# Kernel tuning notes

Hardware: AMD Instinct MI355X
Metric: run time of the kernel (lower is better)

Reference implementation:

```python
import jax, jax.numpy as jnp
import numpy as np

EPS = 1e-9
# exp factors for iterations i = 4,3,2,1,0,-1,-2 ; i == -2 -> 0.0
EXP_FACTORS = np.array([-(4.0 ** i) if i != -2 else 0.0 for i in range(4, -3, -1)], dtype=np.float32)


def setup_inputs() -> dict:
    key = jax.random.key(0)
    k1, k2 = jax.random.split(key)
    B, N, D = 16, 2048, 256
    preds = jax.random.normal(k1, (B, N, D), dtype=jnp.float32)
    labels = jax.random.normal(k2, (B, N, D), dtype=jnp.float32)
    return {"preds": preds, "labels": labels}


def _pairwise_dist(p1, p2):
    # [B,N,1] + [B,1,N] - 2 * p1 @ p2^T -> [B,N,N]
    p1_norm = jnp.sum(p1 * p1, axis=-1)[..., :, None]
    p2_norm = jnp.sum(p2 * p2, axis=-1)[..., None, :]
    return p1_norm + p2_norm - 2.0 * jnp.einsum('bnd,bmd->bnm', p1, p2)


def _approx_match(pwdist):
    B, N, _ = pwdist.shape
    match0 = jnp.zeros_like(pwdist)
    currency0 = jnp.ones((B, N, 1), dtype=pwdist.dtype)
    cost0 = jnp.ones((B, 1, N), dtype=pwdist.dtype)

    def body(carry, exp_factor):
        match, cost, currency = carry
        bids = jnp.exp(exp_factor * pwdist) * cost              # [B,N,N]
        bids = bids * currency / (jnp.sum(bids, axis=2, keepdims=True) + EPS)
        bid_wt = jnp.minimum(cost / (jnp.sum(bids, axis=1, keepdims=True) + EPS), 1.0)
        bids = bids * bid_wt
        match = match + bids
        cost = jnp.maximum(cost - jnp.sum(bids, axis=1, keepdims=True), 0.0)
        currency = jnp.maximum(currency - jnp.sum(bids, axis=2, keepdims=True), 0.0)
        return (match, cost, currency), None

    (match, _, _), _ = jax.lax.scan(body, (match0, cost0, currency0), jnp.asarray(EXP_FACTORS))
    return match


def reference(preds, labels):
    pwdist = _pairwise_dist(preds, labels)
    match = _approx_match(pwdist)
    return jnp.sum(match * pwdist)
```

## Files before the change

kernel.cpp:

```cpp
#include <hip/hip_runtime.h>
#include <cstdint>

#define B_ 16
#define N_ 2048
#define D_ 256
#define EPS_ 1e-9f

#define AS1 __attribute__((address_space(1)))
#define AS3 __attribute__((address_space(3)))

typedef float f4 __attribute__((ext_vector_type(4)));
typedef float f16v __attribute__((ext_vector_type(16)));
typedef int v8i __attribute__((ext_vector_type(8)));

__device__ float blockReduceSum(float x, float* red){
  int tid = threadIdx.x;
  red[tid] = x; __syncthreads();
  #pragma unroll
  for (int off = 128; off > 0; off >>= 1){
    if (tid < off) red[tid] += red[tid + off];
    __syncthreads();
  }
  float r = red[0]; __syncthreads();
  return r;
}

__global__ __launch_bounds__(256) void prep_kernel(
    const float* __restrict__ preds, const float* __restrict__ labels,
    unsigned char* __restrict__ pa8, unsigned char* __restrict__ pb8,
    float* __restrict__ pn, float* __restrict__ ln,
    float* __restrict__ cost, float* __restrict__ currency,
    int* __restrict__ dmin, float* __restrict__ Ppart,
    float* __restrict__ npart, float* __restrict__ out){
  int s = blockIdx.y;
  int tid = threadIdx.x;
  if (s == 0){
    int i = blockIdx.x * 256 + tid;
    if (i < B_ * N_){ cost[i] = 1.f; currency[i] = 1.f; }
    if (i < B_) dmin[i] = 0x7f7fffff;
    if (i == 0) out[0] = 0.f;
  }
  const float* src = s ? labels : preds;
  unsigned char* dst = s ? pb8 : pa8;
  float* norms = s ? ln : pn;
  int w = tid >> 6, lane = tid & 63;
  size_t row0 = (size_t)blockIdx.x * 16 + (size_t)w * 4;
  float4 v[4];
  #pragma unroll
  for (int q = 0; q < 4; q++)
    v[q] = ((const float4*)(src + (row0 + q) * D_))[lane];
  __shared__ f4 part[4][64];
  __shared__ float nred[4];
  f4 s4;
  s4[0] = v[0].x + v[1].x + v[2].x + v[3].x;
  s4[1] = v[0].y + v[1].y + v[2].y + v[3].y;
  s4[2] = v[0].z + v[1].z + v[2].z + v[3].z;
  s4[3] = v[0].w + v[1].w + v[2].w + v[3].w;
  float nsum = 0.f;
  #pragma unroll
  for (int q = 0; q < 4; q++){
    float sum = v[q].x*v[q].x + v[q].y*v[q].y + v[q].z*v[q].z + v[q].w*v[q].w;
    #pragma unroll
    for (int off = 32; off >= 1; off >>= 1) sum += __shfl_xor(sum, off);
    if (lane == 0){ norms[row0 + q] = sum; nsum += sum; }
    int pk = 0;
    pk = __builtin_amdgcn_cvt_pk_fp8_f32(v[q].x, v[q].y, pk, false);
    pk = __builtin_amdgcn_cvt_pk_fp8_f32(v[q].z, v[q].w, pk, true);
    ((unsigned int*)(dst + (row0 + q) * D_))[lane] = (unsigned int)pk;
  }
  part[w][lane] = s4;
  if (lane == 0) nred[w] = nsum;
  __syncthreads();
  if (tid < 64){
    f4 t = part[0][tid];
    #pragma unroll
    for (int q = 1; q < 4; q++){
      t[0] += part[q][tid][0]; t[1] += part[q][tid][1];
      t[2] += part[q][tid][2]; t[3] += part[q][tid][3];
    }
    *(f4*)(Ppart + ((size_t)s * 2048 + blockIdx.x) * 256 + tid * 4) = t;
  }
  if (tid == 0)
    npart[s * 2048 + blockIdx.x] = nred[0] + nred[1] + nred[2] + nred[3];
}

__global__ __launch_bounds__(512, 4) void gemm_minmax(
    const unsigned char* __restrict__ pa, const unsigned char* __restrict__ pbm,
    const float* __restrict__ pn, const float* __restrict__ ln,
    int* __restrict__ dmin)
{
  int lid = blockIdx.x;
  int xcd = lid & 7;
  int l = lid >> 3;
  int b = 2 * xcd + (l >> 5);
  int p = l & 31;
  int tn = (p & 7) * 256;
  int tmb = (p >> 3) * 512;
  const unsigned char* A  = pa  + (size_t)b * N_ * D_;
  const unsigned char* Bm = pbm + (size_t)b * N_ * D_;
  __shared__ __align__(16) unsigned char smem[256 * 256];
  __shared__ float minred[8];
  unsigned char* Bs = smem;
  unsigned char* As0 = smem;
  unsigned char* As1 = smem + 16384;
  float* pnL = (float*)(smem + 32768);
  int tid = threadIdx.x, lane = tid & 63, w = tid >> 6;
  int wm = (w >> 2) * 32, wn = (w & 3) * 64;
  int l31 = lane & 31, half = lane >> 5;
  int rB = lane >> 4, cB = lane & 15;
  const int SC = 0x7F7F7F7F;

  #pragma unroll
  for (int q = 0; q < 8; q++){
    int R = q * 32 + w * 4;
    int r = R + rB;
    int gc = cB ^ (r & 7);
    __builtin_amdgcn_global_load_lds(
        (const AS1 unsigned int*)(const void*)&Bm[(size_t)(tn + r) * D_ + gc * 16],
        (AS3 unsigned int*)(void*)&Bs[R * 256 + lane * 16], 16, 0, 0);
  }

  float lnj[2];
  #pragma unroll
  for (int j = 0; j < 2; j++)
    lnj[j] = ln[(size_t)b * N_ + tn + wn + j * 32 + l31];

  __syncthreads();

  v8i bfr[2][4];
  #pragma unroll
  for (int j = 0; j < 2; j++){
    int rb = wn + j * 32 + l31;
    #pragma unroll
    for (int kc = 0; kc < 4; kc++){
      int c0 = kc * 4 + half * 2;
      int4 lo = *(const int4*)&Bs[rb * 256 + ((c0 ^ (rb & 7)) * 16)];
      int4 hi = *(const int4*)&Bs[rb * 256 + (((c0 + 1) ^ (rb & 7)) * 16)];
      v8i t;
      t[0] = lo.x; t[1] = lo.y; t[2] = lo.z; t[3] = lo.w;
      t[4] = hi.x; t[5] = hi.y; t[6] = hi.z; t[7] = hi.w;
      bfr[j][kc] = t;
    }
  }

  __syncthreads();

  __builtin_amdgcn_global_load_lds(
      (const AS1 unsigned int*)(const void*)&pn[(size_t)b * N_ + tmb + tid],
      (AS3 unsigned int*)(void*)&pnL[tid], 4, 0, 0);
  #pragma unroll
  for (int q = 0; q < 2; q++){
    int R = q * 32 + w * 4;
    int r = R + rB;
    int gc = cB ^ (r & 7);
    __builtin_amdgcn_global_load_lds(
        (const AS1 unsigned int*)(const void*)&A[(size_t)(tmb + r) * D_ + gc * 16],
        (AS3 unsigned int*)(void*)&As0[R * 256 + lane * 16], 16, 0, 0);
  }

  float mind = 3.4e38f;
  int buf = 0;
  for (int step = 0; step < 8; step++){
    __syncthreads();
    unsigned char* Acur = buf ? As1 : As0;
    unsigned char* Anxt = buf ? As0 : As1;
    if (step < 7){
      #pragma unroll
      for (int q = 0; q < 2; q++){
        int R = q * 32 + w * 4;
        int r = R + rB;
        int gc = cB ^ (r & 7);
        __builtin_amdgcn_global_load_lds(
            (const AS1 unsigned int*)(const void*)&A[(size_t)(tmb + (step + 1) * 64 + r) * D_ + gc * 16],
            (AS3 unsigned int*)(void*)&Anxt[R * 256 + lane * 16], 16, 0, 0);
      }
    }
    f16v acc[2];
    acc[0] = (f16v)0.f; acc[1] = (f16v)0.f;

    int ra = wm + l31;
    #pragma unroll
    for (int kc = 0; kc < 4; kc++){
      int c0 = kc * 4 + half * 2;
      int4 lo = *(const int4*)&Acur[ra * 256 + ((c0 ^ (ra & 7)) * 16)];
      int4 hi = *(const int4*)&Acur[ra * 256 + (((c0 + 1) ^ (ra & 7)) * 16)];
      v8i af;
      af[0] = lo.x; af[1] = lo.y; af[2] = lo.z; af[3] = lo.w;
      af[4] = hi.x; af[5] = hi.y; af[6] = hi.z; af[7] = hi.w;
      #pragma unroll
      for (int j = 0; j < 2; j++)
        acc[j] = __builtin_amdgcn_mfma_scale_f32_32x32x64_f8f6f4(
            af, bfr[j][kc], acc[j], 0, 0, 0, SC, 0, SC);
    }

    int prow0 = step * 64 + wm + half * 4;
    #pragma unroll
    for (int h = 0; h < 2; h++){
      float4 p0 = *(const float4*)&pnL[prow0 + h * 16];
      float4 p1 = *(const float4*)&pnL[prow0 + h * 16 + 8];
      float pv[8] = {p0.x, p0.y, p0.z, p0.w, p1.x, p1.y, p1.z, p1.w};
      #pragma unroll
      for (int j = 0; j < 2; j++){
        #pragma unroll
        for (int r8 = 0; r8 < 8; r8++){
          float v = pv[r8] + lnj[j] - 2.f * acc[j][h * 8 + r8];
          mind = fminf(mind, v);
        }
      }
    }
    buf ^= 1;
  }

  #pragma unroll
  for (int off = 32; off >= 1; off >>= 1) mind = fminf(mind, __shfl_xor(mind, off));
  if (lane == 0) minred[w] = mind;
  __syncthreads();
  if (tid == 0){
    float m = minred[0];
    #pragma unroll
    for (int q = 1; q < 8; q++) m = fminf(m, minred[q]);
    atomicMin(&dmin[b], __float_as_int(fmaxf(m, 0.f)));
  }
}

__global__ __launch_bounds__(256) void tail(
    const float* __restrict__ preds, const float* __restrict__ labels,
    const float* __restrict__ pn, const float* __restrict__ ln,
    float* __restrict__ cost, float* __restrict__ currency,
    const int* __restrict__ dmin, const float* __restrict__ Ppart,
    const float* __restrict__ npart, float* __restrict__ out)
{
  const float EF[6] = {-256.f, -64.f, -16.f, -4.f, -1.f, -0.25f};
  int b = blockIdx.x, tid = threadIdx.x;
  float dm = __int_as_float(dmin[b]);
  __shared__ float red[256];

  if (-0.25f * (dm - 16.f) < -55.f){
    float Pc = 0.f, Lc = 0.f;
    for (int k = 0; k < 128; k++){
      Pc += Ppart[((size_t)b * 128 + k) * 256 + tid];
      Lc += Ppart[((size_t)(2048 + b * 128 + k)) * 256 + tid];
    }
    float np = (tid < 128) ? npart[b * 128 + tid] : 0.f;
    float nl = (tid < 128) ? npart[2048 + b * 128 + tid] : 0.f;
    float Spn = blockReduceSum(np, red);
    float Sln = blockReduceSum(nl, red);
    float dot = blockReduceSum(Pc * Lc, red);
    if (tid == 0) atomicAdd(out, Spn + Sln - dot * (1.f / 1024.f));
    return;
  }

  __shared__ float alpha_l[N_];
  __shared__ float prow[D_];
  const float* A  = preds  + (size_t)b * N_ * D_;
  const float* Bm = labels + (size_t)b * N_ * D_;
  const float* pnb = pn + (size_t)b * N_;
  const float* lnb = ln + (size_t)b * N_;
  float* costb = cost + (size_t)b * N_;
  float* curb  = currency + (size_t)b * N_;
  for (int it = 0; it < 6; it++){
    float ef = EF[it];
    if (ef * (dm - 16.f) < -55.f) continue;
    float cost_c[8], colsum_c[8], bw_c[8], costnew_c[8];
    #pragma unroll
    for (int j = 0; j < 8; j++){ cost_c[j] = costb[j*256+tid]; colsum_c[j] = 0.f; }
    for (int r = 0; r < N_; r++){
      prow[tid] = A[(size_t)r * D_ + tid];
      __syncthreads();
      float s_c[8], rs = 0.f;
      for (int j = 0; j < 8; j++){
        int m = j*256+tid; float dot = 0.f;
        for (int k = 0; k < D_; k++) dot += prow[k] * Bm[(size_t)m * D_ + k];
        float d = pnb[r] + lnb[m] - 2.f*dot;
        float s = __expf(ef * d) * cost_c[j];
        s_c[j] = s; rs += s;
      }
      float tot = blockReduceSum(rs, red);
      float a = curb[r] / (tot + EPS_);
      if (tid == 0) alpha_l[r] = a;
      #pragma unroll
      for (int j = 0; j < 8; j++) colsum_c[j] += s_c[j] * a;
      __syncthreads();
    }
    #pragma unroll
    for (int j = 0; j < 8; j++){
      float cs = colsum_c[j];
      float bw = fminf(cost_c[j] / (cs + EPS_), 1.f);
      bw_c[j] = bw; costnew_c[j] = fmaxf(cost_c[j] - bw*cs, 0.f);
    }
    float contrib = 0.f;
    for (int r = 0; r < N_; r++){
      prow[tid] = A[(size_t)r * D_ + tid];
      __syncthreads();
      float a = alpha_l[r], rbs = 0.f;
      for (int j = 0; j < 8; j++){
        int m = j*256+tid; float dot = 0.f;
        for (int k = 0; k < D_; k++) dot += prow[k] * Bm[(size_t)m * D_ + k];
        float d = pnb[r] + lnb[m] - 2.f*dot;
        float bid = __expf(ef * d) * cost_c[j] * a * bw_c[j];
        rbs += bid; contrib += bid * d;
      }
      float tot = blockReduceSum(rbs, red);
      if (tid == 0) curb[r] = fmaxf(curb[r] - tot, 0.f);
      __syncthreads();
    }
    #pragma unroll
    for (int j = 0; j < 8; j++) costb[j*256+tid] = costnew_c[j];
    float ctot = blockReduceSum(contrib, red);
    if (tid == 0) atomicAdd(out, ctot);
    __syncthreads();
  }
  float s = 0.f;
  #pragma unroll
  for (int j = 0; j < 8; j++) s += costb[j*256+tid];
  float Sc = blockReduceSum(s, red);
  float sa = 0.f, spn = 0.f;
  #pragma unroll
  for (int j = 0; j < 8; j++){
    int i = j*256+tid;
    float a = curb[i] / (Sc + EPS_);
    alpha_l[i] = a; sa += a; spn += a * pnb[i];
  }
  float Sa  = blockReduceSum(sa, red);
  float Spn = blockReduceSum(spn, red);
  float Pc = 0.f;
  for (int r = 0; r < N_; r++)
    Pc += alpha_l[r] * A[(size_t)r * D_ + tid];
  __syncthreads();
  float sv = 0.f, sln = 0.f;
  #pragma unroll
  for (int j = 0; j < 8; j++){
    int i = j*256+tid;
    float c = costb[i];
    float bw = fminf(c / (c * Sa + EPS_), 1.f);
    float vv = c * bw;
    alpha_l[i] = vv; sv += vv; sln += vv * lnb[i];
  }
  float Sv  = blockReduceSum(sv, red);
  float Sln = blockReduceSum(sln, red);
  float Lc = 0.f;
  for (int m = 0; m < N_; m++)
    Lc += alpha_l[m] * Bm[(size_t)m * D_ + tid];
  float dot = blockReduceSum(Pc * Lc, red);
  if (tid == 0) atomicAdd(out, Spn * Sv + Sa * Sln - 2.f * dot);
}

extern "C" void kernel_launch(void* const* d_in, const int* in_sizes, int n_in,
                              void* d_out, int out_size, void* d_ws, size_t ws_size,
                              hipStream_t stream)
{
  const float* preds  = (const float*)d_in[0];
  const float* labels = (const float*)d_in[1];
  float* out = (float*)d_out;
  char* ws = (char*)d_ws;
  const size_t BN = (size_t)B_ * N_;
  size_t off = 0;
  float* cost     = (float*)(ws + off); off += BN * 4;
  float* currency = (float*)(ws + off); off += BN * 4;
  float* pn       = (float*)(ws + off); off += BN * 4;
  float* ln       = (float*)(ws + off); off += BN * 4;
  int*   dmin     = (int*)(ws + off);   off += 256;
  float* npart    = (float*)(ws + off); off += (size_t)2 * 2048 * 4;
  float* Ppart    = (float*)(ws + off); off += (size_t)2 * 2048 * 256 * 4;
  unsigned char* pa8 = (unsigned char*)(ws + off); off += BN * D_;
  unsigned char* pb8 = (unsigned char*)(ws + off); off += BN * D_;

  prep_kernel<<<dim3((unsigned)(BN / 16), 2), 256, 0, stream>>>(
      preds, labels, pa8, pb8, pn, ln, cost, currency, dmin, Ppart, npart, out);
  gemm_minmax<<<dim3(512), 512, 0, stream>>>(pa8, pb8, pn, ln, dmin);
  tail<<<dim3(B_), 256, 0, stream>>>(preds, labels, pn, ln, cost, currency, dmin,
                                     Ppart, npart, out);
}
```

Baseline: 141.8 us.

## Restructure fp8 min-distance GEMM: each wave owns one 32-col B slice, 32-row A steps

Reworks the work split in the fp8 MFMA min-distance kernel. Each of the 8 waves now holds a single 32-column B fragment and sweeps 32-row A tiles over 16 steps, instead of a 2x4 wave grid with two fragments and 64-row tiles. B and the A double buffers get separate LDS regions, so the extra sync that let them alias is gone. The pn row norms are now read straight from global memory instead of being staged in LDS. This cuts registers and syncs per step but doubles the number of pipeline steps, lowers MFMA work per barrier, and the larger 80 KB LDS footprint may cap occupancy below the 4 blocks per CU the launch bounds ask for.

```diff
diff --git a/kernel.cpp b/kernel.cpp
--- a/kernel.cpp
+++ b/kernel.cpp
@@ -98,14 +98,11 @@
   int tmb = (p >> 3) * 512;
   const unsigned char* A  = pa  + (size_t)b * N_ * D_;
   const unsigned char* Bm = pbm + (size_t)b * N_ * D_;
-  __shared__ __align__(16) unsigned char smem[256 * 256];
-  __shared__ float minred[8];
-  unsigned char* Bs = smem;
-  unsigned char* As0 = smem;
-  unsigned char* As1 = smem + 16384;
-  float* pnL = (float*)(smem + 32768);
+  __shared__ __align__(16) unsigned char smem[81920];
+  unsigned char* Bs  = smem;
+  unsigned char* As0 = smem + 65536;
+  unsigned char* As1 = smem + 65536 + 8192;
   int tid = threadIdx.x, lane = tid & 63, w = tid >> 6;
-  int wm = (w >> 2) * 32, wn = (w & 3) * 64;
   int l31 = lane & 31, half = lane >> 5;
   int rB = lane >> 4, cB = lane & 15;
   const int SC = 0x7F7F7F7F;
@@ -119,18 +116,21 @@
         (const AS1 unsigned int*)(const void*)&Bm[(size_t)(tn + r) * D_ + gc * 16],
         (AS3 unsigned int*)(void*)&Bs[R * 256 + lane * 16], 16, 0, 0);
   }
-
-  float lnj[2];
-  #pragma unroll
-  for (int j = 0; j < 2; j++)
-    lnj[j] = ln[(size_t)b * N_ + tn + wn + j * 32 + l31];
+  {
+    int r = w * 4 + rB;
+    int gc = cB ^ (r & 7);
+    __builtin_amdgcn_global_load_lds(
+        (const AS1 unsigned int*)(const void*)&A[(size_t)(tmb + r) * D_ + gc * 16],
+        (AS3 unsigned int*)(void*)&As0[(w * 4) * 256 + lane * 16], 16, 0, 0);
+  }
+
+  float lnr = ln[(size_t)b * N_ + tn + w * 32 + l31];
 
   __syncthreads();
 
-  v8i bfr[2][4];
-  #pragma unroll
-  for (int j = 0; j < 2; j++){
-    int rb = wn + j * 32 + l31;
+  v8i bfr[4];
+  {
+    int rb = w * 32 + l31;
     #pragma unroll
     for (int kc = 0; kc < 4; kc++){
       int c0 = kc * 4 + half * 2;
@@ -139,46 +139,25 @@
       v8i t;
       t[0] = lo.x; t[1] = lo.y; t[2] = lo.z; t[3] = lo.w;
       t[4] = hi.x; t[5] = hi.y; t[6] = hi.z; t[7] = hi.w;
-      bfr[j][kc] = t;
-    }
-  }
-
-  __syncthreads();
-
-  __builtin_amdgcn_global_load_lds(
-      (const AS1 unsigned int*)(const void*)&pn[(size_t)b * N_ + tmb + tid],
-      (AS3 unsigned int*)(void*)&pnL[tid], 4, 0, 0);
-  #pragma unroll
-  for (int q = 0; q < 2; q++){
-    int R = q * 32 + w * 4;
-    int r = R + rB;
-    int gc = cB ^ (r & 7);
-    __builtin_amdgcn_global_load_lds(
-        (const AS1 unsigned int*)(const void*)&A[(size_t)(tmb + r) * D_ + gc * 16],
-        (AS3 unsigned int*)(void*)&As0[R * 256 + lane * 16], 16, 0, 0);
+      bfr[kc] = t;
+    }
   }
 
   float mind = 3.4e38f;
   int buf = 0;
-  for (int step = 0; step < 8; step++){
+  for (int step = 0; step < 16; step++){
     __syncthreads();
-    unsigned char* Acur = buf ? As1 : As0;
+    const unsigned char* Acur = buf ? As1 : As0;
     unsigned char* Anxt = buf ? As0 : As1;
-    if (step < 7){
-      #pragma unroll
-      for (int q = 0; q < 2; q++){
-        int R = q * 32 + w * 4;
-        int r = R + rB;
-        int gc = cB ^ (r & 7);
-        __builtin_amdgcn_global_load_lds(
-            (const AS1 unsigned int*)(const void*)&A[(size_t)(tmb + (step + 1) * 64 + r) * D_ + gc * 16],
-            (AS3 unsigned int*)(void*)&Anxt[R * 256 + lane * 16], 16, 0, 0);
-      }
-    }
-    f16v acc[2];
-    acc[0] = (f16v)0.f; acc[1] = (f16v)0.f;
-
-    int ra = wm + l31;
+    if (step < 15){
+      int r = w * 4 + rB;
+      int gc = cB ^ (r & 7);
+      __builtin_amdgcn_global_load_lds(
+          (const AS1 unsigned int*)(const void*)&A[(size_t)(tmb + (step + 1) * 32 + r) * D_ + gc * 16],
+          (AS3 unsigned int*)(void*)&Anxt[(w * 4) * 256 + lane * 16], 16, 0, 0);
+    }
+    f16v acc = (f16v)0.f;
+    int ra = l31;
     #pragma unroll
     for (int kc = 0; kc < 4; kc++){
       int c0 = kc * 4 + half * 2;
@@ -187,25 +166,20 @@
       v8i af;
       af[0] = lo.x; af[1] = lo.y; af[2] = lo.z; af[3] = lo.w;
       af[4] = hi.x; af[5] = hi.y; af[6] = hi.z; af[7] = hi.w;
-      #pragma unroll
-      for (int j = 0; j < 2; j++)
-        acc[j] = __builtin_amdgcn_mfma_scale_f32_32x32x64_f8f6f4(
-            af, bfr[j][kc], acc[j], 0, 0, 0, SC, 0, SC);
-    }
-
-    int prow0 = step * 64 + wm + half * 4;
+      acc = __builtin_amdgcn_mfma_scale_f32_32x32x64_f8f6f4(
+          af, bfr[kc], acc, 0, 0, 0, SC, 0, SC);
+    }
+
+    int prow0 = (int)((size_t)0) + step * 32 + half * 4;
     #pragma unroll
     for (int h = 0; h < 2; h++){
-      float4 p0 = *(const float4*)&pnL[prow0 + h * 16];
-      float4 p1 = *(const float4*)&pnL[prow0 + h * 16 + 8];
+      float4 p0 = *(const float4*)&pn[(size_t)b * N_ + tmb + prow0 + h * 16];
+      float4 p1 = *(const float4*)&pn[(size_t)b * N_ + tmb + prow0 + h * 16 + 8];
       float pv[8] = {p0.x, p0.y, p0.z, p0.w, p1.x, p1.y, p1.z, p1.w};
       #pragma unroll
-      for (int j = 0; j < 2; j++){
-        #pragma unroll
-        for (int r8 = 0; r8 < 8; r8++){
-          float v = pv[r8] + lnj[j] - 2.f * acc[j][h * 8 + r8];
-          mind = fminf(mind, v);
-        }
+      for (int r8 = 0; r8 < 8; r8++){
+        float v = pv[r8] + lnr - 2.f * acc[h * 8 + r8];
+        mind = fminf(mind, v);
       }
     }
     buf ^= 1;
@@ -213,6 +187,7 @@
 
   #pragma unroll
   for (int off = 32; off >= 1; off >>= 1) mind = fminf(mind, __shfl_xor(mind, off));
+  float* minred = (float*)smem;
   if (lane == 0) minred[w] = mind;
   __syncthreads();
   if (tid == 0){
```

After: 127.1 us. -10.4%, faster.
